# Performance work log

Hardware: AMD Instinct MI355X
Metric: run time of the kernel (lower is better)

Reference implementation:

```python
import jax, jax.numpy as jnp
import numpy as np
import math

B, T, C, D = 8, 2048, 1024, 1024
N_LAYER, LAYER_ID = 24, 12


def setup_inputs() -> dict:
    key = jax.random.key(0)
    ks = jax.random.split(key, 5)
    r01 = LAYER_ID / (N_LAYER - 1)
    r10 = 1.0 - LAYER_ID / N_LAYER
    ddd = np.arange(C, dtype=np.float64) / C                      # (C,)
    h = np.arange(D, dtype=np.float64)
    decay_speed = -5 + 8 * (h / (D - 1)) ** (0.7 + 1.3 * r01)     # time_decay init
    zigzag = ((np.arange(D) + 1) % 3 - 1) * 0.5
    time_first = np.log(0.3) + zigzag
    scale = C ** -0.5
    return {
        "x": jax.random.normal(ks[0], (B, T, C), jnp.float32),
        "time_decay": jnp.asarray(decay_speed, jnp.float32),
        "time_first": jnp.asarray(time_first, jnp.float32),
        "time_mix_k": jnp.asarray(ddd ** r10, jnp.float32),
        "time_mix_v": jnp.asarray(ddd ** r10 + 0.3 * r01, jnp.float32),
        "time_mix_r": jnp.asarray(ddd ** (0.5 * r10), jnp.float32),
        "Wk": jax.random.normal(ks[1], (D, C), jnp.float32) * scale,
        "Wv": jax.random.normal(ks[2], (D, C), jnp.float32) * scale,
        "Wr": jax.random.normal(ks[3], (D, C), jnp.float32) * scale,
        "Wo": jax.random.normal(ks[4], (C, D), jnp.float32) * scale,
    }


def _wkv(time_decay, time_first, k, v):
    # wkv_t = (e^{u+k_t} v_t + A_{t-1}) / (e^{u+k_t} + B_{t-1})
    # A_t = e^w A_{t-1} + e^{k_t} v_t ;  B_t likewise with v=1 ;  w = -exp(time_decay)
    # Exactly the math of the original conv1d-with-exp-curve trick, in O(T).
    ew = jnp.exp(-jnp.exp(time_decay))   # (D,)
    eu = jnp.exp(time_first)             # (D,)
    ek = jnp.exp(k)                      # [B,T,D]
    ekv = ek * v

    def step(carry, inp):
        a, b = carry                     # [B,D] each
        ekt, ekvt = inp                  # [B,D] each
        out = (eu * ekvt + a) / (eu * ekt + b)
        return (ew * a + ekvt, ew * b + ekt), out

    init = (jnp.zeros_like(ek[:, 0]), jnp.zeros_like(ek[:, 0]))
    xs = (jnp.swapaxes(ek, 0, 1), jnp.swapaxes(ekv, 0, 1))  # [T,B,D]
    _, out = jax.lax.scan(step, init, xs)
    return jnp.swapaxes(out, 0, 1)       # [B,T,D]


def reference(x, time_decay, time_first, time_mix_k, time_mix_v, time_mix_r, Wk, Wv, Wr, Wo):
    # time_shift: prepend zero row, drop last (ZeroPad2d((0,0,1,-1)))
    xx = jnp.pad(x, ((0, 0), (1, 0), (0, 0)))[:, :-1]
    xk = x * time_mix_k + xx * (1 - time_mix_k)
    xv = x * time_mix_v + xx * (1 - time_mix_v)
    xr = x * time_mix_r + xx * (1 - time_mix_r)
    k = jnp.einsum('btc,dc->btd', xk, Wk)
    v = jnp.einsum('btc,dc->btd', xv, Wv)
    sr = jax.nn.sigmoid(jnp.einsum('btc,dc->btd', xr, Wr))
    rwkv = sr * _wkv(time_decay, time_first, k, v)
    return jnp.einsum('btd,cd->btc', rwkv, Wo)
```

## Files before the change

### kernel.cpp

```cpp
#include <hip/hip_runtime.h>
#include <cstdint>
#include <cstddef>

#define Bb 8
#define Tt 2048
#define Cc 1024
#define Dd 1024
#define Mm (Bb*Tt)
#define CL 64
#define NCH (Tt/CL)


typedef __bf16  bf16x8  __attribute__((ext_vector_type(8)));
typedef float   floatx4 __attribute__((ext_vector_type(4)));

__device__ __forceinline__ ushort f2bf(float f) {
    unsigned u = __float_as_uint(f);
    u = (u + 0x7FFF + ((u >> 16) & 1)) >> 16;
    return (ushort)u;
}
__device__ __forceinline__ float bf2f(ushort u) {
    return __uint_as_float(((unsigned)u) << 16);
}

__device__ __forceinline__ void load_lds16(const void* g, void* l) {
    __builtin_amdgcn_global_load_lds((__attribute__((address_space(1))) void*)(g),
                                     (__attribute__((address_space(3))) void*)(l),
                                     16, 0, 0);
}

__global__ __launch_bounds__(256) void prep_mix3(
        const float* __restrict__ x,
        const float* __restrict__ mk, const float* __restrict__ mv,
        const float* __restrict__ mr,
        ushort* __restrict__ xk, ushort* __restrict__ xv, ushort* __restrict__ xr) {
    int i  = blockIdx.x * 256 + threadIdx.x;
    int cq = i & (Cc / 8 - 1);
    int m  = i >> 7;
    int t  = m & (Tt - 1);
    float xc[8], xp[8];
    *(float4*)&xc[0] = ((const float4*)x)[i * 2];
    *(float4*)&xc[4] = ((const float4*)x)[i * 2 + 1];
    if (t != 0) {
        *(float4*)&xp[0] = ((const float4*)x)[(i - Cc / 8) * 2];
        *(float4*)&xp[4] = ((const float4*)x)[(i - Cc / 8) * 2 + 1];
    } else {
#pragma unroll
        for (int j = 0; j < 8; j++) xp[j] = 0.f;
    }
    float wk[8], wv[8], wr[8];
    *(float4*)&wk[0] = ((const float4*)mk)[cq * 2];
    *(float4*)&wk[4] = ((const float4*)mk)[cq * 2 + 1];
    *(float4*)&wv[0] = ((const float4*)mv)[cq * 2];
    *(float4*)&wv[4] = ((const float4*)mv)[cq * 2 + 1];
    *(float4*)&wr[0] = ((const float4*)mr)[cq * 2];
    *(float4*)&wr[4] = ((const float4*)mr)[cq * 2 + 1];
    ushort ok[8], ov[8], orr[8];
#pragma unroll
    for (int j = 0; j < 8; j++) {
        float d = xc[j] - xp[j];
        ok[j]  = f2bf(xp[j] + d * wk[j]);
        ov[j]  = f2bf(xp[j] + d * wv[j]);
        orr[j] = f2bf(xp[j] + d * wr[j]);
    }
    ((ulonglong2*)xk)[i] = *(const ulonglong2*)ok;
    ((ulonglong2*)xv)[i] = *(const ulonglong2*)ov;
    ((ulonglong2*)xr)[i] = *(const ulonglong2*)orr;
}

__global__ __launch_bounds__(256) void cvt_w(
        const float* __restrict__ wk, const float* __restrict__ wv,
        const float* __restrict__ wr, const float* __restrict__ wo,
        ushort* __restrict__ ok, ushort* __restrict__ ov,
        ushort* __restrict__ orr, ushort* __restrict__ oo) {
    int i = blockIdx.x * 256 + threadIdx.x;
    int sel = i >> 18;
    int j = i & ((1 << 18) - 1);
    const float* s = sel == 0 ? wk : sel == 1 ? wv : sel == 2 ? wr : wo;
    ushort* d      = sel == 0 ? ok : sel == 1 ? ov : sel == 2 ? orr : oo;
    float4 f = ((const float4*)s)[j];
    ushort4 o;
    o.x = f2bf(f.x); o.y = f2bf(f.y); o.z = f2bf(f.z); o.w = f2bf(f.w);
    ((ushort4*)d)[j] = o;
}

struct GemmCore256 {
    floatx4 acc[8][4];
    int quad, fr, wm, wn;

    __device__ __forceinline__ void compute(const __bf16* __restrict__ Ac,
                                            int goff) {
        const __bf16* Bc = Ac + 8192;
        bf16x8 af[8], bfr[4];
#pragma unroll
        for (int mi = 0; mi < 8; mi++)
            af[mi] = *(const bf16x8*)&Ac[(wm + mi * 16 + fr) * 32 + goff];
#pragma unroll
        for (int ni = 0; ni < 4; ni++)
            bfr[ni] = *(const bf16x8*)&Bc[(wn + ni * 16 + fr) * 32 + goff];
        __builtin_amdgcn_s_setprio(1);
#pragma unroll
        for (int mi = 0; mi < 8; mi++)
#pragma unroll
            for (int ni = 0; ni < 4; ni++)
                acc[mi][ni] = __builtin_amdgcn_mfma_f32_16x16x32_bf16(
                    af[mi], bfr[ni], acc[mi][ni], 0, 0, 0);
        __builtin_amdgcn_s_setprio(0);
    }

    __device__ __forceinline__ void run(
            const ushort* __restrict__ A, const ushort* __restrict__ Bw,
            long tm, long tn, int Kdim, __bf16* LDSb) {
        const int tid  = threadIdx.x;
        const int lane = tid & 63;
        quad = lane >> 4;
        fr   = lane & 15;
        const int wave = tid >> 6;
        wm   = (wave >> 1) * 0;
        wm   = (wave >> 1) * 0;
        wm   = (wave & ~1) ? 0 : 0;
        wm   = (wave >> 1) * 32;
        wm   = ((wave >> 1)) * 32;
        wm   = (wave >> 1) * 32;
        {
            const int wave_m = wave >> 1;
            (void)wave_m;
        }
        wm = (wave >> 2) * 128;
        wn = (wave & 3) * 64;
        const int swz  = (fr >> 1) & 3;
        const int goff = (quad ^ swz) * 8;

        const int srow  = tid >> 2;
        const int spart = (tid & 3) ^ ((tid >> 3) & 3);
        const ushort* Ag0 = A + (tm + srow) * (long)Kdim + spart * 8;
        const ushort* Ag1 = Ag0 + 128 * (long)Kdim;
        const ushort* Bg0 = Bw + (tn + srow) * (long)Kdim + spart * 8;
        const ushort* Bg1 = Bg0 + 128 * (long)Kdim;
        const int wlds = wave * 512;

        floatx4 zero = {0.f, 0.f, 0.f, 0.f};
#pragma unroll
        for (int a1 = 0; a1 < 8; a1++)
#pragma unroll
            for (int b1 = 0; b1 < 4; b1++) acc[a1][b1] = zero;

        const int NT = Kdim >> 5;

        {
            __bf16* b0 = LDSb;
            load_lds16(Ag0,      b0 + wlds);
            load_lds16(Ag1,      b0 + 4096  + wlds);
            load_lds16(Bg0,      b0 + 8192  + wlds);
            load_lds16(Bg1,      b0 + 12288 + wlds);
            __bf16* b1 = LDSb + 16384;
            load_lds16(Ag0 + 32, b1 + wlds);
            load_lds16(Ag1 + 32, b1 + 4096  + wlds);
            load_lds16(Bg0 + 32, b1 + 8192  + wlds);
            load_lds16(Bg1 + 32, b1 + 12288 + wlds);
        }

        int bcur = 0, bst = 2;
        for (int T = 0; T < NT - 1; ++T) {
            asm volatile("s_waitcnt vmcnt(4) lgkmcnt(0)" ::: "memory");
            __builtin_amdgcn_s_barrier();
            asm volatile("" ::: "memory");
            if (T < NT - 2) {
                const int kt = (T + 2) << 5;
                __bf16* nb = LDSb + bst * 16384;
                load_lds16(Ag0 + kt, nb + wlds);
                load_lds16(Ag1 + kt, nb + 4096  + wlds);
                load_lds16(Bg0 + kt, nb + 8192  + wlds);
                load_lds16(Bg1 + kt, nb + 12288 + wlds);
            }
            compute(LDSb + bcur * 16384, goff);
            if (++bcur == 3) bcur = 0;
            if (++bst == 3) bst = 0;
        }
        asm volatile("s_waitcnt vmcnt(0) lgkmcnt(0)" ::: "memory");
        __builtin_amdgcn_s_barrier();
        asm volatile("" ::: "memory");
        compute(LDSb + bcur * 16384, goff);
    }
};

__device__ __forceinline__ int xcd_swizzle(int nwg) {
    const int orig  = blockIdx.y * 64 + blockIdx.x;
    const int chunk = nwg >> 3;
    return (orig & 7) * chunk + (orig >> 3);
}

template<int MODE>
__global__ __launch_bounds__(512, 2) void gemm_nt(
        const ushort* __restrict__ A, const ushort* __restrict__ Bw,
        void* __restrict__ Co, int Ndim, int Kdim) {
    __shared__ __attribute__((aligned(16))) __bf16 LDSb[3 * 16384];
    const int swz = xcd_swizzle(gridDim.x * gridDim.y);
    const long tm = (long)(swz & 63) * 256;
    const long tn = (long)(swz >> 6) * 256;
    GemmCore256 g;
    g.run(A, Bw, tm, tn, Kdim, LDSb);
#pragma unroll
    for (int mi = 0; mi < 8; mi++)
#pragma unroll
        for (int ni = 0; ni < 4; ni++)
#pragma unroll
            for (int r = 0; r < 4; r++) {
                long grow = tm + g.wm + mi * 16 + g.quad * 4 + r;
                long gcol = tn + g.wn + ni * 16 + g.fr;
                float v = g.acc[mi][ni][r];
                if (MODE == 2) v = 1.f / (1.f + __expf(-v));
                if (MODE == 0)      ((float*)Co)[grow * Ndim + gcol] = v;
                else if (MODE == 3) ((_Float16*)Co)[grow * Ndim + gcol] = (_Float16)v;
                else                ((ushort*)Co)[grow * Ndim + gcol] = f2bf(v);
            }
}

__global__ __launch_bounds__(512, 2) void gemm3_nt(
        const ushort* __restrict__ xk, const ushort* __restrict__ xv,
        const ushort* __restrict__ xr,
        const ushort* __restrict__ wk, const ushort* __restrict__ wv,
        const ushort* __restrict__ wr,
        _Float16* __restrict__ kb, ushort* __restrict__ vb,
        ushort* __restrict__ sb) {
    __shared__ __attribute__((aligned(16))) __bf16 LDSb[3 * 16384];
    const int swz = xcd_swizzle(64 * 12);
    const int mt  = swz & 63;
    const int yt  = swz >> 6;
    const int proj = yt >> 2;
    const long tm = (long)mt * 256;
    const long tn = (long)(yt & 3) * 256;
    const ushort* A  = proj == 0 ? xk : proj == 1 ? xv : xr;
    const ushort* Bw = proj == 0 ? wk : proj == 1 ? wv : wr;
    GemmCore256 g;
    g.run(A, Bw, tm, tn, Cc, LDSb);
#pragma unroll
    for (int mi = 0; mi < 8; mi++)
#pragma unroll
        for (int ni = 0; ni < 4; ni++)
#pragma unroll
            for (int r = 0; r < 4; r++) {
                long grow = tm + g.wm + mi * 16 + g.quad * 4 + r;
                long gcol = tn + g.wn + ni * 16 + g.fr;
                long off = grow * Dd + gcol;
                float v = g.acc[mi][ni][r];
                if (proj == 0)      kb[off] = (_Float16)v;
                else if (proj == 1) vb[off] = f2bf(v);
                else                sb[off] = f2bf(1.f / (1.f + __expf(-v)));
            }
}

__global__ __launch_bounds__(256) void wkv_part(
        const _Float16* __restrict__ kb, const ushort* __restrict__ vb,
        const float* __restrict__ decay,
        float* __restrict__ pa, float* __restrict__ pb) {
    int gid = blockIdx.x * 256 + threadIdx.x;
    int d = gid & (Dd - 1);
    int c = (gid >> 10) & (NCH - 1);
    int b = gid >> 15;
    float ew = __expf(-__expf(decay[d]));
    size_t base = ((size_t)b * Tt + (size_t)c * CL) * Dd + d;
    float a = 0.f, bs = 0.f;
    for (int i0 = 0; i0 < CL; i0 += 8) {
        float kr[8], vr[8];
#pragma unroll
        for (int j = 0; j < 8; j++) {
            size_t idx = base + (size_t)(i0 + j) * Dd;
            kr[j] = (float)kb[idx]; vr[j] = bf2f(vb[idx]);
        }
#pragma unroll
        for (int j = 0; j < 8; j++) {
            float ek = __expf(kr[j]);
            a  = ew * a  + ek * vr[j];
            bs = ew * bs + ek;
        }
    }
    int sidx = c * (Bb * Dd) + b * Dd + d;
    pa[sidx] = a; pb[sidx] = bs;
}

__global__ __launch_bounds__(256) void wkv_prefix(
        const float* __restrict__ pa, const float* __restrict__ pb,
        const float* __restrict__ decay,
        float* __restrict__ sa, float* __restrict__ sb) {
    int gid = blockIdx.x * 256 + threadIdx.x;
    int d = gid & (Dd - 1);
    float ewL = __expf(-__expf(decay[d]) * (float)CL);
    float ca = 0.f, cb = 0.f;
#pragma unroll
    for (int c = 0; c < NCH; c++) {
        int idx = c * (Bb * Dd) + gid;
        sa[idx] = ca; sb[idx] = cb;
        ca = ewL * ca + pa[idx];
        cb = ewL * cb + pb[idx];
    }
}

__global__ __launch_bounds__(256) void wkv_chunk(
        const _Float16* __restrict__ kb, const ushort* __restrict__ vb,
        const ushort* __restrict__ sr,
        const float* __restrict__ decay, const float* __restrict__ tf,
        const float* __restrict__ sa, const float* __restrict__ sb,
        ushort* __restrict__ rw) {
    int gid = blockIdx.x * 256 + threadIdx.x;
    int d = gid & (Dd - 1);
    int c = (gid >> 10) & (NCH - 1);
    int b = gid >> 15;
    float ew = __expf(-__expf(decay[d]));
    float eu = __expf(tf[d]);
    int sidx = c * (Bb * Dd) + b * Dd + d;
    float a = sa[sidx], bs = sb[sidx];
    size_t base = ((size_t)b * Tt + (size_t)c * CL) * Dd + d;
    for (int i0 = 0; i0 < CL; i0 += 8) {
        float kr[8], vr[8], rr[8];
#pragma unroll
        for (int j = 0; j < 8; j++) {
            size_t idx = base + (size_t)(i0 + j) * Dd;
            kr[j] = (float)kb[idx]; vr[j] = bf2f(vb[idx]); rr[j] = bf2f(sr[idx]);
        }
#pragma unroll
        for (int j = 0; j < 8; j++) {
            float ek  = __expf(kr[j]);
            float ekv = ek * vr[j];
            float out = (eu * ekv + a) / (eu * ek + bs);
            a  = ew * a  + ekv;
            bs = ew * bs + ek;
            rw[base + (size_t)(i0 + j) * Dd] = f2bf(rr[j] * out);
        }
    }
}

extern "C" void kernel_launch(void* const* d_in, const int* in_sizes, int n_in,
                              void* d_out, int out_size, void* d_ws, size_t ws_size,
                              hipStream_t stream) {
    (void)in_sizes; (void)n_in; (void)out_size;
    const float* x  = (const float*)d_in[0];
    const float* td = (const float*)d_in[1];
    const float* tf = (const float*)d_in[2];
    const float* mk = (const float*)d_in[3];
    const float* mv = (const float*)d_in[4];
    const float* mr = (const float*)d_in[5];
    const float* Wk = (const float*)d_in[6];
    const float* Wv = (const float*)d_in[7];
    const float* Wr = (const float*)d_in[8];
    const float* Wo = (const float*)d_in[9];
    float* out = (float*)d_out;

    const size_t xsz = (size_t)Mm * Cc * 2;
    const size_t wsz = (size_t)Dd * Cc * 2;
    const size_t ssz = (size_t)Bb * NCH * Dd * 4;
    const size_t need_merged = 6 * xsz + 4 * wsz + 4 * ssz;

    char* p = (char*)d_ws;
    auto take = [&](size_t n) { char* r = p; p += n; return r; };
    ushort*   xk = (ushort*)take(xsz);
    ushort*   xv = (ushort*)take(xsz);
    ushort*   xr = (ushort*)take(xsz);
    _Float16* kb = (_Float16*)take(xsz);
    const bool merged = ws_size >= need_merged;
    ushort *vb, *sb, *rw;
    if (merged) {
        vb = (ushort*)take(xsz);
        sb = (ushort*)take(xsz);
        rw = xk;
    } else {
        vb = xk;
        sb = xv;
        rw = xr;
    }
    ushort* wk = (ushort*)take(wsz);
    ushort* wv = (ushort*)take(wsz);
    ushort* wr = (ushort*)take(wsz);
    ushort* wo = (ushort*)take(wsz);
    float*  pa = (float*)take(ssz);
    float*  pb = (float*)take(ssz);
    float*  sa = (float*)take(ssz);
    float*  sbst = (float*)take(ssz);

    dim3 g1(Mm / 256, Dd / 256);
    dim3 g2(Mm / 256, Cc / 256);
    dim3 g3(Mm / 256, 3 * Dd / 256);
    const int wkv_grid = (Bb * NCH * Dd) / 256;

    cvt_w<<<4096, 256, 0, stream>>>(Wk, Wv, Wr, Wo, wk, wv, wr, wo);
    prep_mix3<<<Mm * Cc / 8 / 256, 256, 0, stream>>>(x, mk, mv, mr, xk, xv, xr);

    if (merged) {
        gemm3_nt<<<g3, 512, 0, stream>>>(xk, xv, xr, wk, wv, wr, kb, vb, sb);
    } else {
        gemm_nt<3><<<g1, 512, 0, stream>>>(xk, wk, kb, Dd, Cc);
        gemm_nt<1><<<g1, 512, 0, stream>>>(xv, wv, vb, Dd, Cc);
        gemm_nt<2><<<g1, 512, 0, stream>>>(xr, wr, sb, Dd, Cc);
    }

    wkv_part  <<<wkv_grid, 256, 0, stream>>>(kb, vb, td, pa, pb);
    wkv_prefix<<<(Bb * Dd) / 256, 256, 0, stream>>>(pa, pb, td, sa, sbst);
    wkv_chunk <<<wkv_grid, 256, 0, stream>>>(kb, vb, sb, td, tf, sa, sbst, rw);

    gemm_nt<0><<<g2, 512, 0, stream>>>(rw, wo, out, Cc, Dd);
}
```

Measured before the change: 386.9 us.

## Restructure GEMM core into 8-phase ping-pong schedule with K=64 tiles

Replaces the triple-buffered K=32 GEMM mainloop with a double-buffered K=64 loop split into four barrier-separated phases. Each phase interleaves a small set of LDS fragment reads with MFMA groups, and the LDS swizzle is widened to 8 groups. The block-to-tile mapping is also changed so each XCD gets a contiguous range of M tiles. The aim is to overlap LDS reads, global-to-LDS loads and MFMA across the waves and to halve the number of loop iterations. The cost is many more barriers per iteration and a larger 128KB LDS footprint, which may limit occupancy to two blocks per CU.

```diff
diff --git a/kernel.cpp b/kernel.cpp
--- a/kernel.cpp
+++ b/kernel.cpp
@@ -14,6 +14,8 @@
 typedef __bf16  bf16x8  __attribute__((ext_vector_type(8)));
 typedef float   floatx4 __attribute__((ext_vector_type(4)));
 
+#define MFMA16(a, b, c) __builtin_amdgcn_mfma_f32_16x16x32_bf16((a), (b), (c), 0, 0, 0)
+
 __device__ __forceinline__ ushort f2bf(float f) {
     unsigned u = __float_as_uint(f);
     u = (u + 0x7FFF + ((u >> 16) & 1)) >> 16;
@@ -28,6 +30,9 @@
                                      (__attribute__((address_space(3))) void*)(l),
                                      16, 0, 0);
 }
+
+#define CFENCE asm volatile("" ::: "memory")
+#define BARRIER do { CFENCE; __builtin_amdgcn_s_barrier(); CFENCE; } while (0)
 
 __global__ __launch_bounds__(256) void prep_mix3(
         const float* __restrict__ x,
@@ -84,29 +89,9 @@
     ((ushort4*)d)[j] = o;
 }
 
-struct GemmCore256 {
+struct Gemm8P {
     floatx4 acc[8][4];
     int quad, fr, wm, wn;
-
-    __device__ __forceinline__ void compute(const __bf16* __restrict__ Ac,
-                                            int goff) {
-        const __bf16* Bc = Ac + 8192;
-        bf16x8 af[8], bfr[4];
-#pragma unroll
-        for (int mi = 0; mi < 8; mi++)
-            af[mi] = *(const bf16x8*)&Ac[(wm + mi * 16 + fr) * 32 + goff];
-#pragma unroll
-        for (int ni = 0; ni < 4; ni++)
-            bfr[ni] = *(const bf16x8*)&Bc[(wn + ni * 16 + fr) * 32 + goff];
-        __builtin_amdgcn_s_setprio(1);
-#pragma unroll
-        for (int mi = 0; mi < 8; mi++)
-#pragma unroll
-            for (int ni = 0; ni < 4; ni++)
-                acc[mi][ni] = __builtin_amdgcn_mfma_f32_16x16x32_bf16(
-                    af[mi], bfr[ni], acc[mi][ni], 0, 0, 0);
-        __builtin_amdgcn_s_setprio(0);
-    }
 
     __device__ __forceinline__ void run(
             const ushort* __restrict__ A, const ushort* __restrict__ Bw,
@@ -116,99 +101,159 @@
         quad = lane >> 4;
         fr   = lane & 15;
         const int wave = tid >> 6;
-        wm   = (wave >> 1) * 0;
-        wm   = (wave >> 1) * 0;
-        wm   = (wave & ~1) ? 0 : 0;
-        wm   = (wave >> 1) * 32;
-        wm   = ((wave >> 1)) * 32;
-        wm   = (wave >> 1) * 32;
-        {
-            const int wave_m = wave >> 1;
-            (void)wave_m;
-        }
         wm = (wave >> 2) * 128;
         wn = (wave & 3) * 64;
-        const int swz  = (fr >> 1) & 3;
-        const int goff = (quad ^ swz) * 8;
-
-        const int srow  = tid >> 2;
-        const int spart = (tid & 3) ^ ((tid >> 3) & 3);
-        const ushort* Ag0 = A + (tm + srow) * (long)Kdim + spart * 8;
-        const ushort* Ag1 = Ag0 + 128 * (long)Kdim;
-        const ushort* Bg0 = Bw + (tn + srow) * (long)Kdim + spart * 8;
-        const ushort* Bg1 = Bg0 + 128 * (long)Kdim;
+        const int x7 = fr & 7;
+        const int g0 = (quad ^ x7) * 8;
+        const int g1 = ((4 + quad) ^ x7) * 8;
+
+        const int srow = tid >> 3;
+        const int scol = ((tid & 7) ^ (srow & 7)) * 8;
         const int wlds = wave * 512;
 
+        const ushort* Ag[4]; const ushort* Bg[4];
+#pragma unroll
+        for (int j = 0; j < 4; j++) {
+            Ag[j] = A  + (tm + j * 64 + srow) * (long)Kdim + scol;
+            Bg[j] = Bw + (tn + j * 64 + srow) * (long)Kdim + scol;
+        }
+
+        auto stage = [&](__bf16* buf, long koff) {
+#pragma unroll
+            for (int j = 0; j < 4; j++) {
+                load_lds16(Ag[j] + koff, buf + j * 4096 + wlds);
+                load_lds16(Bg[j] + koff, buf + 16384 + j * 4096 + wlds);
+            }
+        };
+
         floatx4 zero = {0.f, 0.f, 0.f, 0.f};
 #pragma unroll
-        for (int a1 = 0; a1 < 8; a1++)
-#pragma unroll
-            for (int b1 = 0; b1 < 4; b1++) acc[a1][b1] = zero;
-
-        const int NT = Kdim >> 5;
-
-        {
-            __bf16* b0 = LDSb;
-            load_lds16(Ag0,      b0 + wlds);
-            load_lds16(Ag1,      b0 + 4096  + wlds);
-            load_lds16(Bg0,      b0 + 8192  + wlds);
-            load_lds16(Bg1,      b0 + 12288 + wlds);
-            __bf16* b1 = LDSb + 16384;
-            load_lds16(Ag0 + 32, b1 + wlds);
-            load_lds16(Ag1 + 32, b1 + 4096  + wlds);
-            load_lds16(Bg0 + 32, b1 + 8192  + wlds);
-            load_lds16(Bg1 + 32, b1 + 12288 + wlds);
-        }
-
-        int bcur = 0, bst = 2;
-        for (int T = 0; T < NT - 1; ++T) {
-            asm volatile("s_waitcnt vmcnt(4) lgkmcnt(0)" ::: "memory");
-            __builtin_amdgcn_s_barrier();
-            asm volatile("" ::: "memory");
-            if (T < NT - 2) {
-                const int kt = (T + 2) << 5;
-                __bf16* nb = LDSb + bst * 16384;
-                load_lds16(Ag0 + kt, nb + wlds);
-                load_lds16(Ag1 + kt, nb + 4096  + wlds);
-                load_lds16(Bg0 + kt, nb + 8192  + wlds);
-                load_lds16(Bg1 + kt, nb + 12288 + wlds);
-            }
-            compute(LDSb + bcur * 16384, goff);
-            if (++bcur == 3) bcur = 0;
-            if (++bst == 3) bst = 0;
-        }
-        asm volatile("s_waitcnt vmcnt(0) lgkmcnt(0)" ::: "memory");
-        __builtin_amdgcn_s_barrier();
-        asm volatile("" ::: "memory");
-        compute(LDSb + bcur * 16384, goff);
+        for (int ai = 0; ai < 8; ai++)
+#pragma unroll
+            for (int nj = 0; nj < 4; nj++) acc[ai][nj] = zero;
+
+        const int NT = Kdim >> 6;
+
+        stage(LDSb, 0);
+        if (NT > 1) {
+            stage(LDSb + 32768, 64);
+            asm volatile("s_waitcnt vmcnt(8)" ::: "memory");
+        } else {
+            asm volatile("s_waitcnt vmcnt(0)" ::: "memory");
+        }
+        BARRIER;
+
+        bf16x8 a0[4][2], a1[4][2], b0[2][2], b1[2][2];
+
+        for (int T = 0; T < NT; ++T) {
+            const __bf16* Ab = LDSb + (T & 1) * 32768;
+            const __bf16* Bbf = Ab + 16384;
+
+#pragma unroll
+            for (int mi = 0; mi < 4; mi++) {
+                const __bf16* p = &Ab[(wm + mi * 16 + fr) * 64];
+                a0[mi][0] = *(const bf16x8*)(p + g0);
+                a0[mi][1] = *(const bf16x8*)(p + g1);
+            }
+#pragma unroll
+            for (int ni = 0; ni < 2; ni++) {
+                const __bf16* p = &Bbf[(wn + ni * 16 + fr) * 64];
+                b0[ni][0] = *(const bf16x8*)(p + g0);
+                b0[ni][1] = *(const bf16x8*)(p + g1);
+            }
+            if (T >= 1 && T + 1 < NT)
+                stage(LDSb + ((T + 1) & 1) * 32768, (long)(T + 1) * 64);
+            BARRIER;
+            __builtin_amdgcn_s_setprio(1);
+#pragma unroll
+            for (int mi = 0; mi < 4; mi++)
+#pragma unroll
+                for (int ni = 0; ni < 2; ni++) {
+                    acc[mi][ni] = MFMA16(a0[mi][0], b0[ni][0], acc[mi][ni]);
+                    acc[mi][ni] = MFMA16(a0[mi][1], b0[ni][1], acc[mi][ni]);
+                }
+            __builtin_amdgcn_s_setprio(0);
+            BARRIER;
+
+#pragma unroll
+            for (int ni = 0; ni < 2; ni++) {
+                const __bf16* p = &Bbf[(wn + 32 + ni * 16 + fr) * 64];
+                b1[ni][0] = *(const bf16x8*)(p + g0);
+                b1[ni][1] = *(const bf16x8*)(p + g1);
+            }
+            BARRIER;
+            __builtin_amdgcn_s_setprio(1);
+#pragma unroll
+            for (int mi = 0; mi < 4; mi++)
+#pragma unroll
+                for (int ni = 0; ni < 2; ni++) {
+                    acc[mi][2 + ni] = MFMA16(a0[mi][0], b1[ni][0], acc[mi][2 + ni]);
+                    acc[mi][2 + ni] = MFMA16(a0[mi][1], b1[ni][1], acc[mi][2 + ni]);
+                }
+            __builtin_amdgcn_s_setprio(0);
+            BARRIER;
+
+#pragma unroll
+            for (int mi = 0; mi < 4; mi++) {
+                const __bf16* p = &Ab[(wm + 64 + mi * 16 + fr) * 64];
+                a1[mi][0] = *(const bf16x8*)(p + g0);
+                a1[mi][1] = *(const bf16x8*)(p + g1);
+            }
+            BARRIER;
+            __builtin_amdgcn_s_setprio(1);
+#pragma unroll
+            for (int mi = 0; mi < 4; mi++)
+#pragma unroll
+                for (int ni = 0; ni < 2; ni++) {
+                    acc[4 + mi][2 + ni] = MFMA16(a1[mi][0], b1[ni][0], acc[4 + mi][2 + ni]);
+                    acc[4 + mi][2 + ni] = MFMA16(a1[mi][1], b1[ni][1], acc[4 + mi][2 + ni]);
+                }
+            __builtin_amdgcn_s_setprio(0);
+            BARRIER;
+
+#pragma unroll
+            for (int ni = 0; ni < 2; ni++) {
+                const __bf16* p = &Bbf[(wn + ni * 16 + fr) * 64];
+                b0[ni][0] = *(const bf16x8*)(p + g0);
+                b0[ni][1] = *(const bf16x8*)(p + g1);
+            }
+            if (T + 1 < NT)
+                asm volatile("s_waitcnt vmcnt(0)" ::: "memory");
+            BARRIER;
+            __builtin_amdgcn_s_setprio(1);
+#pragma unroll
+            for (int mi = 0; mi < 4; mi++)
+#pragma unroll
+                for (int ni = 0; ni < 2; ni++) {
+                    acc[4 + mi][ni] = MFMA16(a1[mi][0], b0[ni][0], acc[4 + mi][ni]);
+                    acc[4 + mi][ni] = MFMA16(a1[mi][1], b0[ni][1], acc[4 + mi][ni]);
+                }
+            __builtin_amdgcn_s_setprio(0);
+            BARRIER;
+        }
     }
 };
-
-__device__ __forceinline__ int xcd_swizzle(int nwg) {
-    const int orig  = blockIdx.y * 64 + blockIdx.x;
-    const int chunk = nwg >> 3;
-    return (orig & 7) * chunk + (orig >> 3);
-}
 
 template<int MODE>
 __global__ __launch_bounds__(512, 2) void gemm_nt(
         const ushort* __restrict__ A, const ushort* __restrict__ Bw,
         void* __restrict__ Co, int Ndim, int Kdim) {
-    __shared__ __attribute__((aligned(16))) __bf16 LDSb[3 * 16384];
-    const int swz = xcd_swizzle(gridDim.x * gridDim.y);
-    const long tm = (long)(swz & 63) * 256;
-    const long tn = (long)(swz >> 6) * 256;
-    GemmCore256 g;
+    __shared__ __attribute__((aligned(16))) __bf16 LDSb[2 * 32768];
+    const int orig = blockIdx.y * 64 + blockIdx.x;
+    const int L    = (orig & 7) * 32 + (orig >> 3);
+    const long tm = (long)(L >> 2) * 256;
+    const long tn = (long)(L & 3) * 256;
+    Gemm8P g;
     g.run(A, Bw, tm, tn, Kdim, LDSb);
 #pragma unroll
-    for (int mi = 0; mi < 8; mi++)
-#pragma unroll
-        for (int ni = 0; ni < 4; ni++)
+    for (int ai = 0; ai < 8; ai++)
+#pragma unroll
+        for (int nj = 0; nj < 4; nj++)
 #pragma unroll
             for (int r = 0; r < 4; r++) {
-                long grow = tm + g.wm + mi * 16 + g.quad * 4 + r;
-                long gcol = tn + g.wn + ni * 16 + g.fr;
-                float v = g.acc[mi][ni][r];
+                long grow = tm + g.wm + ai * 16 + g.quad * 4 + r;
+                long gcol = tn + g.wn + nj * 16 + g.fr;
+                float v = g.acc[ai][nj][r];
                 if (MODE == 2) v = 1.f / (1.f + __expf(-v));
                 if (MODE == 0)      ((float*)Co)[grow * Ndim + gcol] = v;
                 else if (MODE == 3) ((_Float16*)Co)[grow * Ndim + gcol] = (_Float16)v;
@@ -223,27 +268,27 @@
         const ushort* __restrict__ wr,
         _Float16* __restrict__ kb, ushort* __restrict__ vb,
         ushort* __restrict__ sb) {
-    __shared__ __attribute__((aligned(16))) __bf16 LDSb[3 * 16384];
-    const int swz = xcd_swizzle(64 * 12);
-    const int mt  = swz & 63;
-    const int yt  = swz >> 6;
-    const int proj = yt >> 2;
-    const long tm = (long)mt * 256;
-    const long tn = (long)(yt & 3) * 256;
+    __shared__ __attribute__((aligned(16))) __bf16 LDSb[2 * 32768];
+    const int orig = blockIdx.y * 64 + blockIdx.x;
+    const int L    = (orig & 7) * 96 + (orig >> 3);
+    const int proj = L >> 8;
+    const int rem  = L & 255;
+    const long tm = (long)(rem >> 2) * 256;
+    const long tn = (long)(rem & 3) * 256;
     const ushort* A  = proj == 0 ? xk : proj == 1 ? xv : xr;
     const ushort* Bw = proj == 0 ? wk : proj == 1 ? wv : wr;
-    GemmCore256 g;
+    Gemm8P g;
     g.run(A, Bw, tm, tn, Cc, LDSb);
 #pragma unroll
-    for (int mi = 0; mi < 8; mi++)
-#pragma unroll
-        for (int ni = 0; ni < 4; ni++)
+    for (int ai = 0; ai < 8; ai++)
+#pragma unroll
+        for (int nj = 0; nj < 4; nj++)
 #pragma unroll
             for (int r = 0; r < 4; r++) {
-                long grow = tm + g.wm + mi * 16 + g.quad * 4 + r;
-                long gcol = tn + g.wn + ni * 16 + g.fr;
+                long grow = tm + g.wm + ai * 16 + g.quad * 4 + r;
+                long gcol = tn + g.wn + nj * 16 + g.fr;
                 long off = grow * Dd + gcol;
-                float v = g.acc[mi][ni][r];
+                float v = g.acc[ai][nj][r];
                 if (proj == 0)      kb[off] = (_Float16)v;
                 else if (proj == 1) vb[off] = f2bf(v);
                 else                sb[off] = f2bf(1.f / (1.f + __expf(-v)));
```

Result: no change. 380.7 us (-1.6%).
